# Optimization experiments

Hardware: AMD Instinct MI355X
Metric: run time of the kernel (lower is better)

Reference implementation:

```python
import jax, jax.numpy as jnp
import numpy as np

B, L, H, NH = 4, 2048, 2048, 16
HD = H // NH  # head_dim = 128


def setup_inputs() -> dict:
    key = jax.random.key(0)
    ks = jax.random.split(key, 5)
    x = jax.random.normal(ks[0], (B, L, H), dtype=jnp.float32)
    Wqkv = jax.random.normal(ks[1], (H, 3 * H), dtype=jnp.float32) * (1.0 / np.sqrt(H))
    bqkv = jnp.zeros((3 * H,), dtype=jnp.float32)
    Wfc2 = jax.random.normal(ks[2], (H, H), dtype=jnp.float32) * (1.0 / np.sqrt(H))
    bfc2 = jnp.zeros((H,), dtype=jnp.float32)
    # RoPE tables over the FULL hidden dim (as in the torch module)
    inv_freq = 1.0 / (10000.0 ** (jnp.arange(0, H, 2, dtype=jnp.float32) / H))  # [H/2]
    t = jnp.arange(L, dtype=jnp.float32)
    freqs = jnp.outer(t, inv_freq)  # [L, H/2]
    return {"x": x, "Wqkv": Wqkv, "bqkv": bqkv, "Wfc2": Wfc2, "bfc2": bfc2,
            "cos": jnp.cos(freqs), "sin": jnp.sin(freqs)}


def _apply_rotary(u, cos, sin):
    # u: [b, l, H]; rotate halves over full hidden dim
    l = u.shape[1]
    d = u.shape[-1] // 2
    u1, u2 = u[..., :d], u[..., d:]
    c, s = cos[:l], sin[:l]  # [l, d] broadcast over batch
    return jnp.concatenate([u1 * c + u2 * s, -u1 * s + u2 * c], axis=-1)


def reference(x, Wqkv, bqkv, Wfc2, bfc2, cos, sin):
    b, l, _ = x.shape
    qkv = x @ Wqkv + bqkv  # [b, l, 3H]
    q, k, v = jnp.split(qkv, 3, axis=-1)
    q = _apply_rotary(q, cos, sin)
    k = _apply_rotary(k, cos, sin)
    # NOTE: heads are the FASTEST axis in the original view(b, l, head_dim, heads)
    def to_heads(u):
        return jnp.transpose(u.reshape(b, l, HD, NH), (0, 3, 1, 2))  # [b, h, l, d]
    q, k, v = to_heads(q), to_heads(k), to_heads(v)
    scale = 1.0 / np.sqrt(HD)
    scores = jnp.einsum('bhqd,bhkd->bhqk', q, k) * scale
    causal = jnp.tril(jnp.ones((l, l), dtype=bool))
    scores = jnp.where(causal, scores, jnp.finfo(scores.dtype).min)
    p = jax.nn.softmax(scores, axis=-1)
    y = jnp.einsum('bhqk,bhkd->bhqd', p, v)
    y = jnp.transpose(y, (0, 2, 1, 3)).reshape(b, l, H)  # [b, l, h*d]
    return jax.nn.silu(y @ Wfc2 + bfc2)
```

## Files before the change

kernel.cpp:

```cpp
#include <hip/hip_runtime.h>
#include <hip/hip_bf16.h>
#include <cstdint>
#include <cstddef>


typedef __attribute__((ext_vector_type(4))) float f32x4;
typedef __attribute__((ext_vector_type(8))) short bf16x8;
typedef __hip_bfloat16 bf16;

#define ASYNC16(lds, g)                                                                  \
  __builtin_amdgcn_global_load_lds((const __attribute__((address_space(1))) void*)(g),   \
                                   (__attribute__((address_space(3))) void*)(lds), 16, 0, 0)

__device__ __forceinline__ float b2f(bf16 v) { return __bfloat162float(v); }
__device__ __forceinline__ bf16 f2b(float v) { return __float2bfloat16(v); }
__device__ __forceinline__ short f2bs(float f) {
  bf16 h = __float2bfloat16(f);
  return __builtin_bit_cast(short, h);
}
__device__ __forceinline__ bf16x8 pack8(f32x4 a, f32x4 b) {
  bf16x8 r;
#pragma unroll
  for (int t = 0; t < 4; ++t) r[t] = f2bs(a[t]);
#pragma unroll
  for (int t = 0; t < 4; ++t) r[4 + t] = f2bs(b[t]);
  return r;
}

template <int CTRL>
__device__ __forceinline__ float dpp_bfly_max(float x) {
  int xi = __builtin_bit_cast(int, x);
  int yi = __builtin_amdgcn_update_dpp(xi, xi, CTRL, 0xF, 0xF, false);
  return fmaxf(x, __builtin_bit_cast(float, yi));
}
template <int CTRL>
__device__ __forceinline__ float dpp_bfly_add(float x) {
  int xi = __builtin_bit_cast(int, x);
  int yi = __builtin_amdgcn_update_dpp(xi, xi, CTRL, 0xF, 0xF, false);
  return x + __builtin_bit_cast(float, yi);
}

__global__ void conv_bf16(const float* __restrict__ src, bf16* __restrict__ dst) {
  size_t i = ((size_t)blockIdx.x * 256 + threadIdx.x) * 8;
  f32x4 a0 = *(const f32x4*)(src + i);
  f32x4 a1 = *(const f32x4*)(src + i + 4);
  *(bf16x8*)(dst + i) = pack8(a0, a1);
}

__global__ void transpose_conv(const float* __restrict__ src, bf16* __restrict__ dst,
                               int R, int C, int perm) {
  __shared__ float tile[32][33];
  int bx = blockIdx.x * 32, by = blockIdx.y * 32;
  int tx = threadIdx.x, ty = threadIdx.y;
  for (int i = ty; i < 32; i += 8) tile[i][tx] = src[(size_t)(by + i) * C + bx + tx];
  __syncthreads();
  for (int i = ty; i < 32; i += 8) {
    int c = bx + i;
    if (perm) {
      int cc = c & 2047;
      c = (c & ~2047) | (((cc & 15) << 7) | (cc >> 4));
    }
    dst[(size_t)c * R + by + tx] = f2b(tile[tx][i]);
  }
}

__global__ __launch_bounds__(256) void gemm_qkv(const bf16* __restrict__ A,
                                                const bf16* __restrict__ Bt,
                                                const float* __restrict__ biasf,
                                                bf16* __restrict__ Qg, bf16* __restrict__ Kg,
                                                bf16* __restrict__ Vg) {
  __shared__ alignas(16) bf16 smem[2 * 128 * 64];
  bf16* As = smem;
  bf16* Bs = smem + 128 * 64;
  const int K_ = 2048;
  int tid = threadIdx.x, lane = tid & 63, w = tid >> 6;
  int lr = lane & 15, hi = lane >> 4;
  int wm = (w >> 1) * 64, wn = (w & 1) * 64;
  int m0 = blockIdx.y * 128, n0 = blockIdx.x * 128;
  f32x4 acc[4][4];
#pragma unroll
  for (int im = 0; im < 4; ++im)
#pragma unroll
    for (int in = 0; in < 4; ++in) acc[im][in] = (f32x4){0.f, 0.f, 0.f, 0.f};

  for (int k0 = 0; k0 < K_; k0 += 64) {
    __syncthreads();
#pragma unroll
    for (int i = 0; i < 4; ++i) {
      int c = tid + 256 * i;
      int r = c >> 3, j = c & 7, jg = j ^ (r & 7);
      ASYNC16((char*)As + c * 16, (const char*)(A + (size_t)(m0 + r) * K_ + k0 + jg * 8));
    }
#pragma unroll
    for (int i = 0; i < 4; ++i) {
      int c = tid + 256 * i;
      int r = c >> 3, j = c & 7, jg = j ^ (r & 7);
      ASYNC16((char*)Bs + c * 16, (const char*)(Bt + (size_t)(n0 + r) * K_ + k0 + jg * 8));
    }
    __syncthreads();

#pragma unroll
    for (int ks = 0; ks < 2; ++ks) {
      bf16x8 afr[4], bfr[4];
#pragma unroll
      for (int im = 0; im < 4; ++im) {
        int r = wm + 16 * im + lr;
        afr[im] = *(const bf16x8*)((const char*)As + r * 128 + (((ks * 4 + hi) ^ (r & 7)) * 16));
      }
#pragma unroll
      for (int in = 0; in < 4; ++in) {
        int r = wn + 16 * in + lr;
        bfr[in] = *(const bf16x8*)((const char*)Bs + r * 128 + (((ks * 4 + hi) ^ (r & 7)) * 16));
      }
#pragma unroll
      for (int im = 0; im < 4; ++im)
#pragma unroll
        for (int in = 0; in < 4; ++in)
          acc[im][in] =
              __builtin_amdgcn_mfma_f32_16x16x32_bf16(afr[im], bfr[in], acc[im][in], 0, 0, 0);
    }
  }

  int which = n0 >> 11;
  int h = (n0 >> 7) & 15;
  int bq = m0 >> 11;
  int l_base = m0 & 2047;
  int bh = bq * 16 + h;
  float bv[4];
#pragma unroll
  for (int in = 0; in < 4; ++in)
    bv[in] = biasf[(which << 11) + ((wn + 16 * in + lr) << 4) + h];

  if (which < 2) {
    bf16* __restrict__ G = (which == 0) ? Qg : Kg;
#pragma unroll
    for (int im = 0; im < 4; ++im) {
#pragma unroll
      for (int in = 0; in < 4; ++in) {
        int d = wn + 16 * in + lr;
#pragma unroll
        for (int j = 0; j < 4; ++j) {
          int l = l_base + wm + 16 * im + 4 * hi + j;
          G[((size_t)bh * 2048 + l) * 128 + d] = f2b(acc[im][in][j] + bv[in]);
        }
      }
    }
  } else {
    __syncthreads();
#pragma unroll
    for (int im = 0; im < 4; ++im)
#pragma unroll
      for (int in = 0; in < 4; ++in) {
        int d = wn + 16 * in + lr;
#pragma unroll
        for (int j = 0; j < 4; ++j) {
          int l = wm + 16 * im + 4 * hi + j;
          int slot = (l >> 3) ^ (d & 15);
          smem[d * 128 + slot * 8 + (l & 7)] = f2b(acc[im][in][j] + bv[in]);
        }
      }
    __syncthreads();
#pragma unroll
    for (int s = 0; s < 8; ++s) {
      int d = (tid >> 4) + 16 * s;
      int lc = tid & 15;
      int slot = lc ^ (d & 15);
      bf16x8 v = *(const bf16x8*)(smem + d * 128 + slot * 8);
      *(bf16x8*)(Vg + ((size_t)bh * 128 + d) * 2048 + l_base + lc * 8) = v;
    }
  }
}

__global__ __launch_bounds__(256) void gemm_fc2(const bf16* __restrict__ A,
                                                const bf16* __restrict__ Bt,
                                                const float* __restrict__ biasf,
                                                float* __restrict__ Out) {
  __shared__ alignas(16) bf16 As[128 * 64];
  __shared__ alignas(16) bf16 Bs[128 * 64];
  const int K_ = 2048;
  int tid = threadIdx.x, lane = tid & 63, w = tid >> 6;
  int lr = lane & 15, hi = lane >> 4;
  int wm = (w >> 1) * 64, wn = (w & 1) * 64;
  int m0 = blockIdx.y * 128, n0 = blockIdx.x * 128;
  f32x4 acc[4][4];
#pragma unroll
  for (int im = 0; im < 4; ++im)
#pragma unroll
    for (int in = 0; in < 4; ++in) acc[im][in] = (f32x4){0.f, 0.f, 0.f, 0.f};

  for (int k0 = 0; k0 < K_; k0 += 64) {
    __syncthreads();
#pragma unroll
    for (int i = 0; i < 4; ++i) {
      int c = tid + 256 * i;
      int r = c >> 3, j = c & 7, jg = j ^ (r & 7);
      ASYNC16((char*)As + c * 16, (const char*)(A + (size_t)(m0 + r) * K_ + k0 + jg * 8));
    }
#pragma unroll
    for (int i = 0; i < 4; ++i) {
      int c = tid + 256 * i;
      int r = c >> 3, j = c & 7, jg = j ^ (r & 7);
      ASYNC16((char*)Bs + c * 16, (const char*)(Bt + (size_t)(n0 + r) * K_ + k0 + jg * 8));
    }
    __syncthreads();
#pragma unroll
    for (int ks = 0; ks < 2; ++ks) {
      bf16x8 afr[4], bfr[4];
#pragma unroll
      for (int im = 0; im < 4; ++im) {
        int r = wm + 16 * im + lr;
        afr[im] = *(const bf16x8*)((const char*)As + r * 128 + (((ks * 4 + hi) ^ (r & 7)) * 16));
      }
#pragma unroll
      for (int in = 0; in < 4; ++in) {
        int r = wn + 16 * in + lr;
        bfr[in] = *(const bf16x8*)((const char*)Bs + r * 128 + (((ks * 4 + hi) ^ (r & 7)) * 16));
      }
#pragma unroll
      for (int im = 0; im < 4; ++im)
#pragma unroll
        for (int in = 0; in < 4; ++in)
          acc[im][in] =
              __builtin_amdgcn_mfma_f32_16x16x32_bf16(afr[im], bfr[in], acc[im][in], 0, 0, 0);
    }
  }

#pragma unroll
  for (int im = 0; im < 4; ++im) {
#pragma unroll
    for (int in = 0; in < 4; ++in) {
      int c = n0 + wn + 16 * in + lr;
      float bv = biasf[c];
#pragma unroll
      for (int j = 0; j < 4; ++j) {
        int m = m0 + wm + 16 * im + 4 * hi + j;
        float z = acc[im][in][j] + bv;
        Out[(size_t)m * 2048 + c] = z / (1.f + __expf(-z));
      }
    }
  }
}

__global__ void rotary_kernel(bf16* __restrict__ Qg, bf16* __restrict__ Kg,
                              const float* __restrict__ cosp, const float* __restrict__ sinp) {
  int idx = blockIdx.x * 256 + threadIdx.x;
  int d = idx & 63;
  int l = (idx >> 6) & 2047;
  int bh = idx >> 17;
  int h = bh & 15;
  size_t base = ((size_t)bh * 2048 + l) * 128;
  int ang = l * 1024 + d * 16 + h;
  float c = cosp[ang], s = sinp[ang];
  float q1 = b2f(Qg[base + d]), q2 = b2f(Qg[base + d + 64]);
  Qg[base + d] = f2b(q1 * c + q2 * s);
  Qg[base + d + 64] = f2b(-q1 * s + q2 * c);
  float k1 = b2f(Kg[base + d]), k2 = b2f(Kg[base + d + 64]);
  Kg[base + d] = f2b(k1 * c + k2 * s);
  Kg[base + d + 64] = f2b(-k1 * s + k2 * c);
}

__global__ __launch_bounds__(256) void flash_kernel(const bf16* __restrict__ Qg,
                                                    const bf16* __restrict__ Kg,
                                                    const bf16* __restrict__ Vg,
                                                    bf16* __restrict__ Y) {
  __shared__ alignas(16) bf16 Ks[64 * 128];
  __shared__ alignas(16) bf16 Vt[128 * 64];
  __shared__ alignas(16) bf16 Ps[4 * 16 * 72];
  int tid = threadIdx.x, lane = tid & 63, w = tid >> 6;
  int lr = lane & 15, hi = lane >> 4;
  int it = 31 - (int)blockIdx.x;
  int bh = blockIdx.y;
  int b = bh >> 4, h = bh & 15;
  int q0 = it * 64;
  const bf16* Qb = Qg + (size_t)bh * 2048 * 128;
  const bf16* Kb = Kg + (size_t)bh * 2048 * 128;
  const bf16* Vb = Vg + (size_t)bh * 128 * 2048;
  const float NEG = -1.0e30f;
  int ar = 16 * w + lr;

  bf16x8 qf[4];
#pragma unroll
  for (int ks = 0; ks < 4; ++ks)
    qf[ks] = *(const bf16x8*)(Qb + (size_t)(q0 + ar) * 128 + (ks * 4 + hi) * 8);

  bf16x8 kreg[4], vreg[4];
#pragma unroll
  for (int i = 0; i < 4; ++i) {
    int c = tid + 256 * i;
    int rk = c >> 4, jk = (c & 15) ^ (rk & 7);
    kreg[i] = *(const bf16x8*)(Kb + (size_t)rk * 128 + jk * 8);
    int rv = c >> 3, jv = (c & 7) ^ (rv & 7);
    vreg[i] = *(const bf16x8*)(Vb + (size_t)rv * 2048 + jv * 8);
  }

  f32x4 o[8];
#pragma unroll
  for (int i = 0; i < 8; ++i) o[i] = (f32x4){0.f, 0.f, 0.f, 0.f};
  float m_i[4], l_i[4];
#pragma unroll
  for (int j = 0; j < 4; ++j) { m_i[j] = NEG; l_i[j] = 0.f; }
  const float scale = 0.08838834764831845f;

  for (int jt = 0; jt <= it; ++jt) {
    __syncthreads();
#pragma unroll
    for (int i = 0; i < 4; ++i) {
      int c = tid + 256 * i;
      *(bf16x8*)((char*)Ks + c * 16) = kreg[i];
      *(bf16x8*)((char*)Vt + c * 16) = vreg[i];
    }
    __syncthreads();

    if (jt < it) {
      int k0n = (jt + 1) * 64;
#pragma unroll
      for (int i = 0; i < 4; ++i) {
        int c = tid + 256 * i;
        int rk = c >> 4, jk = (c & 15) ^ (rk & 7);
        kreg[i] = *(const bf16x8*)(Kb + (size_t)(k0n + rk) * 128 + jk * 8);
        int rv = c >> 3, jv = (c & 7) ^ (rv & 7);
        vreg[i] = *(const bf16x8*)(Vb + (size_t)rv * 2048 + k0n + jv * 8);
      }
    }

    f32x4 sacc[4];
#pragma unroll
    for (int in = 0; in < 4; ++in) sacc[in] = (f32x4){0.f, 0.f, 0.f, 0.f};
#pragma unroll
    for (int ks = 0; ks < 4; ++ks) {
#pragma unroll
      for (int in = 0; in < 4; ++in) {
        int br = 16 * in + lr;
        bf16x8 bb =
            *(const bf16x8*)((const char*)Ks + br * 256 + (((ks * 4 + hi) ^ (br & 7)) * 16));
        sacc[in] = __builtin_amdgcn_mfma_f32_16x16x32_bf16(qf[ks], bb, sacc[in], 0, 0, 0);
      }
    }

    bool diag = (jt == it);
    float mxr[4], alpha[4], rsum[4];
#pragma unroll
    for (int j = 0; j < 4; ++j) {
      float mx = NEG;
#pragma unroll
      for (int in = 0; in < 4; ++in) {
        float s = sacc[in][j] * scale;
        if (diag) {
          int qg = 16 * w + 4 * hi + j;
          int kg = 16 * in + lr;
          if (kg > qg) s = NEG;
        }
        sacc[in][j] = s;
        mx = fmaxf(mx, s);
      }
      mxr[j] = mx;
    }
#pragma unroll
    for (int j = 0; j < 4; ++j) mxr[j] = dpp_bfly_max<0xB1>(mxr[j]);
#pragma unroll
    for (int j = 0; j < 4; ++j) mxr[j] = dpp_bfly_max<0x4E>(mxr[j]);
#pragma unroll
    for (int j = 0; j < 4; ++j) mxr[j] = dpp_bfly_max<0x141>(mxr[j]);
#pragma unroll
    for (int j = 0; j < 4; ++j) mxr[j] = dpp_bfly_max<0x140>(mxr[j]);

#pragma unroll
    for (int j = 0; j < 4; ++j) {
      float mnew = fmaxf(m_i[j], mxr[j]);
      alpha[j] = __expf(m_i[j] - mnew);
      m_i[j] = mnew;
      float r = 0.f;
#pragma unroll
      for (int in = 0; in < 4; ++in) {
        float p = __expf(sacc[in][j] - mnew);
        sacc[in][j] = p;
        r += p;
      }
      rsum[j] = r;
    }
#pragma unroll
    for (int j = 0; j < 4; ++j) rsum[j] = dpp_bfly_add<0xB1>(rsum[j]);
#pragma unroll
    for (int j = 0; j < 4; ++j) rsum[j] = dpp_bfly_add<0x4E>(rsum[j]);
#pragma unroll
    for (int j = 0; j < 4; ++j) rsum[j] = dpp_bfly_add<0x141>(rsum[j]);
#pragma unroll
    for (int j = 0; j < 4; ++j) rsum[j] = dpp_bfly_add<0x140>(rsum[j]);

#pragma unroll
    for (int j = 0; j < 4; ++j) {
      l_i[j] = alpha[j] * l_i[j] + rsum[j];
#pragma unroll
      for (int inp = 0; inp < 8; ++inp) o[inp][j] *= alpha[j];
    }

#pragma unroll
    for (int j = 0; j < 4; ++j)
#pragma unroll
      for (int in = 0; in < 4; ++in)
        Ps[w * 1152 + (4 * hi + j) * 72 + 16 * in + lr] = f2b(sacc[in][j]);
    asm volatile("s_waitcnt lgkmcnt(0)" ::: "memory");

#pragma unroll
    for (int ko = 0; ko < 2; ++ko) {
      bf16x8 a = *(const bf16x8*)((const char*)Ps + (w * 1152 + lr * 72 + ko * 32 + hi * 8) * 2);
#pragma unroll
      for (int inp = 0; inp < 8; ++inp) {
        int br = 16 * inp + lr;
        bf16x8 bb =
            *(const bf16x8*)((const char*)Vt + br * 128 + (((ko * 4 + hi) ^ (br & 7)) * 16));
        o[inp] = __builtin_amdgcn_mfma_f32_16x16x32_bf16(a, bb, o[inp], 0, 0, 0);
      }
    }
  }

#pragma unroll
  for (int j = 0; j < 4; ++j) {
    int qg = q0 + 16 * w + 4 * hi + j;
    float inv = 1.f / l_i[j];
    size_t rowb = ((size_t)(b * 2048 + qg)) * 2048 + h * 128;
#pragma unroll
    for (int inp = 0; inp < 8; ++inp) {
      int dd = 16 * inp + lr;
      Y[rowb + dd] = f2b(o[inp][j] * inv);
    }
  }
}

extern "C" void kernel_launch(void* const* d_in, const int* in_sizes, int n_in,
                              void* d_out, int out_size, void* d_ws, size_t ws_size,
                              hipStream_t stream) {
  const float* x    = (const float*)d_in[0];
  const float* Wqkv = (const float*)d_in[1];
  const float* bqkv = (const float*)d_in[2];
  const float* Wfc2 = (const float*)d_in[3];
  const float* bfc2 = (const float*)d_in[4];
  const float* cosp = (const float*)d_in[5];
  const float* sinp = (const float*)d_in[6];
  float* out = (float*)d_out;

  bf16* ws = (bf16*)d_ws;
  bf16* Yg    = ws;
  bf16* WqkvT = ws;
  bf16* Qg    = ws + 16777216;
  bf16* Wfc2T = ws + 16777216;
  bf16* Kg    = ws + 33554432;
  bf16* Vg    = ws + 50331648;
  bf16* xb    = (bf16*)d_out;

  conv_bf16<<<8192, 256, 0, stream>>>(x, xb);
  transpose_conv<<<dim3(192, 64), dim3(32, 8), 0, stream>>>(Wqkv, WqkvT, 2048, 6144, 1);
  gemm_qkv<<<dim3(48, 64), 256, 0, stream>>>(xb, WqkvT, bqkv, Qg, Kg, Vg);
  rotary_kernel<<<32768, 256, 0, stream>>>(Qg, Kg, cosp, sinp);
  flash_kernel<<<dim3(32, 64), 256, 0, stream>>>(Qg, Kg, Vg, Yg);
  transpose_conv<<<dim3(64, 64), dim3(32, 8), 0, stream>>>(Wfc2, Wfc2T, 2048, 2048, 0);
  gemm_fc2<<<dim3(16, 64), 256, 0, stream>>>(Yg, Wfc2T, bfc2, out);
}
```

Measured before the change: 820.2 us.

## Process two 64-row query groups per flash block to reuse K/V tiles

Each flash attention block now handles 128 query rows as two 64-row groups that share every K/V tile staged in LDS, and the grid is halved. This halves global K/V loads and LDS staging per query row. The cost is doubled accumulator and Q register state, which may lower occupancy, plus a final tile where the first group sits idle. With half as many blocks, load balance over the causal triangle is also coarser.

```diff
diff --git a/kernel.cpp b/kernel.cpp
--- a/kernel.cpp
+++ b/kernel.cpp
@@ -265,23 +265,25 @@
                                                     bf16* __restrict__ Y) {
   __shared__ alignas(16) bf16 Ks[64 * 128];
   __shared__ alignas(16) bf16 Vt[128 * 64];
-  __shared__ alignas(16) bf16 Ps[4 * 16 * 72];
+  __shared__ alignas(16) bf16 Ps[4 * 32 * 72];
   int tid = threadIdx.x, lane = tid & 63, w = tid >> 6;
   int lr = lane & 15, hi = lane >> 4;
-  int it = 31 - (int)blockIdx.x;
+  int it = 15 - (int)blockIdx.x;
   int bh = blockIdx.y;
   int b = bh >> 4, h = bh & 15;
-  int q0 = it * 64;
+  int q0 = it * 128;
   const bf16* Qb = Qg + (size_t)bh * 2048 * 128;
   const bf16* Kb = Kg + (size_t)bh * 2048 * 128;
   const bf16* Vb = Vg + (size_t)bh * 128 * 2048;
   const float NEG = -1.0e30f;
   int ar = 16 * w + lr;
 
-  bf16x8 qf[4];
-#pragma unroll
-  for (int ks = 0; ks < 4; ++ks)
-    qf[ks] = *(const bf16x8*)(Qb + (size_t)(q0 + ar) * 128 + (ks * 4 + hi) * 8);
+  bf16x8 qf[2][4];
+#pragma unroll
+  for (int g = 0; g < 2; ++g)
+#pragma unroll
+    for (int ks = 0; ks < 4; ++ks)
+      qf[g][ks] = *(const bf16x8*)(Qb + (size_t)(q0 + 64 * g + ar) * 128 + (ks * 4 + hi) * 8);
 
   bf16x8 kreg[4], vreg[4];
 #pragma unroll
@@ -293,15 +295,20 @@
     vreg[i] = *(const bf16x8*)(Vb + (size_t)rv * 2048 + jv * 8);
   }
 
-  f32x4 o[8];
-#pragma unroll
-  for (int i = 0; i < 8; ++i) o[i] = (f32x4){0.f, 0.f, 0.f, 0.f};
-  float m_i[4], l_i[4];
-#pragma unroll
-  for (int j = 0; j < 4; ++j) { m_i[j] = NEG; l_i[j] = 0.f; }
+  f32x4 o[2][8];
+#pragma unroll
+  for (int g = 0; g < 2; ++g)
+#pragma unroll
+    for (int i = 0; i < 8; ++i) o[g][i] = (f32x4){0.f, 0.f, 0.f, 0.f};
+  float m_i[2][4], l_i[2][4];
+#pragma unroll
+  for (int g = 0; g < 2; ++g)
+#pragma unroll
+    for (int j = 0; j < 4; ++j) { m_i[g][j] = NEG; l_i[g][j] = 0.f; }
   const float scale = 0.08838834764831845f;
 
-  for (int jt = 0; jt <= it; ++jt) {
+  int jt_max = 2 * it + 1;
+  for (int jt = 0; jt <= jt_max; ++jt) {
     __syncthreads();
 #pragma unroll
     for (int i = 0; i < 4; ++i) {
@@ -311,7 +318,7 @@
     }
     __syncthreads();
 
-    if (jt < it) {
+    if (jt < jt_max) {
       int k0n = (jt + 1) * 64;
 #pragma unroll
       for (int i = 0; i < 4; ++i) {
@@ -323,9 +330,11 @@
       }
     }
 
-    f32x4 sacc[4];
-#pragma unroll
-    for (int in = 0; in < 4; ++in) sacc[in] = (f32x4){0.f, 0.f, 0.f, 0.f};
+    f32x4 sacc[2][4];
+#pragma unroll
+    for (int g = 0; g < 2; ++g)
+#pragma unroll
+      for (int in = 0; in < 4; ++in) sacc[g][in] = (f32x4){0.f, 0.f, 0.f, 0.f};
 #pragma unroll
     for (int ks = 0; ks < 4; ++ks) {
 #pragma unroll
@@ -333,98 +342,111 @@
         int br = 16 * in + lr;
         bf16x8 bb =
             *(const bf16x8*)((const char*)Ks + br * 256 + (((ks * 4 + hi) ^ (br & 7)) * 16));
-        sacc[in] = __builtin_amdgcn_mfma_f32_16x16x32_bf16(qf[ks], bb, sacc[in], 0, 0, 0);
-      }
-    }
-
-    bool diag = (jt == it);
-    float mxr[4], alpha[4], rsum[4];
-#pragma unroll
-    for (int j = 0; j < 4; ++j) {
-      float mx = NEG;
-#pragma unroll
-      for (int in = 0; in < 4; ++in) {
-        float s = sacc[in][j] * scale;
-        if (diag) {
-          int qg = 16 * w + 4 * hi + j;
-          int kg = 16 * in + lr;
-          if (kg > qg) s = NEG;
+        if (jt <= 2 * it)
+          sacc[0][in] = __builtin_amdgcn_mfma_f32_16x16x32_bf16(qf[0][ks], bb, sacc[0][in], 0, 0, 0);
+        sacc[1][in] = __builtin_amdgcn_mfma_f32_16x16x32_bf16(qf[1][ks], bb, sacc[1][in], 0, 0, 0);
+      }
+    }
+
+#pragma unroll
+    for (int g = 0; g < 2; ++g) {
+      if (jt > 2 * it + g) continue;
+      bool diag = (jt == 2 * it + g);
+      float mxr[4], alpha[4], rsum[4];
+#pragma unroll
+      for (int j = 0; j < 4; ++j) {
+        float mx = NEG;
+#pragma unroll
+        for (int in = 0; in < 4; ++in) {
+          float s = sacc[g][in][j] * scale;
+          if (diag) {
+            int qg_ = 16 * w + 4 * hi + j;
+            int kg_ = 16 * in + lr;
+            if (kg_ > qg_) s = NEG;
+          }
+          sacc[g][in][j] = s;
+          mx = fmaxf(mx, s);
         }
-        sacc[in][j] = s;
-        mx = fmaxf(mx, s);
-      }
-      mxr[j] = mx;
-    }
-#pragma unroll
-    for (int j = 0; j < 4; ++j) mxr[j] = dpp_bfly_max<0xB1>(mxr[j]);
-#pragma unroll
-    for (int j = 0; j < 4; ++j) mxr[j] = dpp_bfly_max<0x4E>(mxr[j]);
-#pragma unroll
-    for (int j = 0; j < 4; ++j) mxr[j] = dpp_bfly_max<0x141>(mxr[j]);
-#pragma unroll
-    for (int j = 0; j < 4; ++j) mxr[j] = dpp_bfly_max<0x140>(mxr[j]);
-
-#pragma unroll
-    for (int j = 0; j < 4; ++j) {
-      float mnew = fmaxf(m_i[j], mxr[j]);
-      alpha[j] = __expf(m_i[j] - mnew);
-      m_i[j] = mnew;
-      float r = 0.f;
-#pragma unroll
-      for (int in = 0; in < 4; ++in) {
-        float p = __expf(sacc[in][j] - mnew);
-        sacc[in][j] = p;
-        r += p;
-      }
-      rsum[j] = r;
-    }
-#pragma unroll
-    for (int j = 0; j < 4; ++j) rsum[j] = dpp_bfly_add<0xB1>(rsum[j]);
-#pragma unroll
-    for (int j = 0; j < 4; ++j) rsum[j] = dpp_bfly_add<0x4E>(rsum[j]);
-#pragma unroll
-    for (int j = 0; j < 4; ++j) rsum[j] = dpp_bfly_add<0x141>(rsum[j]);
-#pragma unroll
-    for (int j = 0; j < 4; ++j) rsum[j] = dpp_bfly_add<0x140>(rsum[j]);
-
-#pragma unroll
-    for (int j = 0; j < 4; ++j) {
-      l_i[j] = alpha[j] * l_i[j] + rsum[j];
-#pragma unroll
-      for (int inp = 0; inp < 8; ++inp) o[inp][j] *= alpha[j];
-    }
-
-#pragma unroll
-    for (int j = 0; j < 4; ++j)
-#pragma unroll
-      for (int in = 0; in < 4; ++in)
-        Ps[w * 1152 + (4 * hi + j) * 72 + 16 * in + lr] = f2b(sacc[in][j]);
+        mxr[j] = mx;
+      }
+#pragma unroll
+      for (int j = 0; j < 4; ++j) mxr[j] = dpp_bfly_max<0xB1>(mxr[j]);
+#pragma unroll
+      for (int j = 0; j < 4; ++j) mxr[j] = dpp_bfly_max<0x4E>(mxr[j]);
+#pragma unroll
+      for (int j = 0; j < 4; ++j) mxr[j] = dpp_bfly_max<0x141>(mxr[j]);
+#pragma unroll
+      for (int j = 0; j < 4; ++j) mxr[j] = dpp_bfly_max<0x140>(mxr[j]);
+
+#pragma unroll
+      for (int j = 0; j < 4; ++j) {
+        float mnew = fmaxf(m_i[g][j], mxr[j]);
+        alpha[j] = __expf(m_i[g][j] - mnew);
+        m_i[g][j] = mnew;
+        float r = 0.f;
+#pragma unroll
+        for (int in = 0; in < 4; ++in) {
+          float p = __expf(sacc[g][in][j] - mnew);
+          sacc[g][in][j] = p;
+          r += p;
+        }
+        rsum[j] = r;
+      }
+#pragma unroll
+      for (int j = 0; j < 4; ++j) rsum[j] = dpp_bfly_add<0xB1>(rsum[j]);
+#pragma unroll
+      for (int j = 0; j < 4; ++j) rsum[j] = dpp_bfly_add<0x4E>(rsum[j]);
+#pragma unroll
+      for (int j = 0; j < 4; ++j) rsum[j] = dpp_bfly_add<0x141>(rsum[j]);
+#pragma unroll
+      for (int j = 0; j < 4; ++j) rsum[j] = dpp_bfly_add<0x140>(rsum[j]);
+
+#pragma unroll
+      for (int j = 0; j < 4; ++j) {
+        l_i[g][j] = alpha[j] * l_i[g][j] + rsum[j];
+#pragma unroll
+        for (int inp = 0; inp < 8; ++inp) o[g][inp][j] *= alpha[j];
+      }
+
+#pragma unroll
+      for (int j = 0; j < 4; ++j)
+#pragma unroll
+        for (int in = 0; in < 4; ++in)
+          Ps[w * 2304 + (g * 16 + 4 * hi + j) * 72 + 16 * in + lr] = f2b(sacc[g][in][j]);
+    }
     asm volatile("s_waitcnt lgkmcnt(0)" ::: "memory");
 
 #pragma unroll
     for (int ko = 0; ko < 2; ++ko) {
-      bf16x8 a = *(const bf16x8*)((const char*)Ps + (w * 1152 + lr * 72 + ko * 32 + hi * 8) * 2);
+      bf16x8 a0, a1;
+      if (jt <= 2 * it)
+        a0 = *(const bf16x8*)((const char*)Ps + (w * 2304 + lr * 72 + ko * 32 + hi * 8) * 2);
+      a1 = *(const bf16x8*)((const char*)Ps + (w * 2304 + (16 + lr) * 72 + ko * 32 + hi * 8) * 2);
 #pragma unroll
       for (int inp = 0; inp < 8; ++inp) {
         int br = 16 * inp + lr;
         bf16x8 bb =
             *(const bf16x8*)((const char*)Vt + br * 128 + (((ko * 4 + hi) ^ (br & 7)) * 16));
-        o[inp] = __builtin_amdgcn_mfma_f32_16x16x32_bf16(a, bb, o[inp], 0, 0, 0);
-      }
-    }
-  }
-
-#pragma unroll
-  for (int j = 0; j < 4; ++j) {
-    int qg = q0 + 16 * w + 4 * hi + j;
-    float inv = 1.f / l_i[j];
-    size_t rowb = ((size_t)(b * 2048 + qg)) * 2048 + h * 128;
-#pragma unroll
-    for (int inp = 0; inp < 8; ++inp) {
-      int dd = 16 * inp + lr;
-      Y[rowb + dd] = f2b(o[inp][j] * inv);
-    }
-  }
+        if (jt <= 2 * it)
+          o[0][inp] = __builtin_amdgcn_mfma_f32_16x16x32_bf16(a0, bb, o[0][inp], 0, 0, 0);
+        o[1][inp] = __builtin_amdgcn_mfma_f32_16x16x32_bf16(a1, bb, o[1][inp], 0, 0, 0);
+      }
+    }
+  }
+
+#pragma unroll
+  for (int g = 0; g < 2; ++g)
+#pragma unroll
+    for (int j = 0; j < 4; ++j) {
+      int qg_ = q0 + 64 * g + 16 * w + 4 * hi + j;
+      float inv = 1.f / l_i[g][j];
+      size_t rowb = ((size_t)(b * 2048 + qg_)) * 2048 + h * 128;
+#pragma unroll
+      for (int inp = 0; inp < 8; ++inp) {
+        int dd = 16 * inp + lr;
+        Y[rowb + dd] = f2b(o[g][inp][j] * inv);
+      }
+    }
 }
 
 extern "C" void kernel_launch(void* const* d_in, const int* in_sizes, int n_in,
@@ -452,7 +474,7 @@
   transpose_conv<<<dim3(192, 64), dim3(32, 8), 0, stream>>>(Wqkv, WqkvT, 2048, 6144, 1);
   gemm_qkv<<<dim3(48, 64), 256, 0, stream>>>(xb, WqkvT, bqkv, Qg, Kg, Vg);
   rotary_kernel<<<32768, 256, 0, stream>>>(Qg, Kg, cosp, sinp);
-  flash_kernel<<<dim3(32, 64), 256, 0, stream>>>(Qg, Kg, Vg, Yg);
+  flash_kernel<<<dim3(16, 64), 256, 0, stream>>>(Qg, Kg, Vg, Yg);
   transpose_conv<<<dim3(64, 64), dim3(32, 8), 0, stream>>>(Wfc2, Wfc2T, 2048, 2048, 0);
   gemm_fc2<<<dim3(16, 64), 256, 0, stream>>>(Yg, Wfc2T, bfc2, out);
 }
```

After: 916.4 us. +11.7%, slower.
